# Kernel optimization log

Hardware: AMD Instinct MI355X
Metric: run time of the kernel (lower is better)

The kernel has to match this reference:

```python
import jax, jax.numpy as jnp
import numpy as np

N = 100000
E = 1600000
D = 128
L = 3  # num_layers
EPS = 1e-5


def setup_inputs() -> dict:
    key = jax.random.key(0)
    ks = jax.random.split(key, 10)
    feat = jax.random.normal(ks[0], (N, D), dtype=jnp.float32)
    src = jax.random.randint(ks[1], (E,), 0, N, dtype=jnp.int32)
    dst = jax.random.randint(ks[2], (E,), 0, N, dtype=jnp.int32)
    s = 1.0 / np.sqrt(D)
    W_pool = jax.random.uniform(ks[3], (L, D, D), jnp.float32, -s, s)
    b_pool = jax.random.uniform(ks[4], (L, D), jnp.float32, -s, s)
    W_self = jax.random.uniform(ks[5], (L, D, D), jnp.float32, -s, s)
    W_neigh = jax.random.uniform(ks[6], (L, D, D), jnp.float32, -s, s)
    bias = jnp.zeros((L, D), jnp.float32)
    gamma = jnp.ones((L, D), jnp.float32)
    beta = jnp.zeros((L, D), jnp.float32)
    return {"feat": feat, "W_pool": W_pool, "b_pool": b_pool, "W_self": W_self,
            "W_neigh": W_neigh, "bias": bias, "gamma": gamma, "beta": beta,
            "src": src, "dst": dst}


def _sage_pool_layer(h, Wp, bp, Ws, Wn, b, src_all, dst_all):
    # DGL SAGEConv(aggregator_type='pool'):
    # h_pool = relu(fc_pool(h)); neigh = max over in-edges of h_pool[src];
    # out = fc_self(h) + fc_neigh(neigh) + bias  (fc_self/fc_neigh bias-free)
    hp = jax.nn.relu(h @ Wp + bp)                      # [N, d]
    msgs = hp[src_all]                                  # [E+N, d] gather
    neigh = jax.ops.segment_max(msgs, dst_all, num_segments=N)  # [N, d]
    return h @ Ws + neigh @ Wn + b


def _bn_relu(x, g, b):
    # BatchNorm1d in training mode (batch stats, biased variance) + ReLU
    mean = jnp.mean(x, axis=0)
    var = jnp.mean(jnp.square(x - mean), axis=0)
    return jax.nn.relu((x - mean) * jax.lax.rsqrt(var + EPS) * g + b)


def reference(feat, W_pool, b_pool, W_self, W_neigh, bias, gamma, beta, src, dst):
    # dgl.add_self_loop
    loop = jnp.arange(N, dtype=src.dtype)
    src_all = jnp.concatenate([src, loop])
    dst_all = jnp.concatenate([dst, loop])
    h = feat
    for l in range(L):
        h = _sage_pool_layer(h, W_pool[l], b_pool[l], W_self[l], W_neigh[l],
                             bias[l], src_all, dst_all)
        h = _bn_relu(h, gamma[l], beta[l])
    return h
```

## Files before the change

### kernel.cpp

```cpp
#include <hip/hip_runtime.h>

#define DD 128
#define MAXB 256
#define BSH 9
#define PEB 4096
#define RB 64
#define CAP 10240

typedef unsigned short u16;
typedef unsigned int   u32;
typedef __attribute__((ext_vector_type(8))) short bf16x8;
typedef __attribute__((ext_vector_type(4))) float f32x4;

union U8 { uint4 u; bf16x8 v; };

__device__ inline u16 f2bf(float x) {
  u32 u = __float_as_uint(x);
  u += 0x7fffu + ((u >> 16) & 1u);
  return (u16)(u >> 16);
}
__device__ inline float bf2f_lo(u32 w) { return __uint_as_float(w << 16); }
__device__ inline float bf2f_hi(u32 w) { return __uint_as_float(w & 0xffff0000u); }

__device__ inline u32 pkmax(u32 a, u32 b) {
  u32 r;
  asm("v_pk_max_u16 %0, %1, %2" : "=v"(r) : "v"(a), "v"(b));
  return r;
}

__device__ inline uint4 fragF32(const float* __restrict__ p) {
  float4 a = *(const float4*)p;
  float4 b = *(const float4*)(p + 4);
  uint4 o;
  o.x = (u32)f2bf(a.x) | ((u32)f2bf(a.y) << 16);
  o.y = (u32)f2bf(a.z) | ((u32)f2bf(a.w) << 16);
  o.z = (u32)f2bf(b.x) | ((u32)f2bf(b.y) << 16);
  o.w = (u32)f2bf(b.z) | ((u32)f2bf(b.w) << 16);
  return o;
}

__device__ inline uint4 fragBN(const u16* __restrict__ p,
                               const float* __restrict__ sc,
                               const float* __restrict__ sh, int k0) {
  uint4 u = *(const uint4*)p;
  float4 c0 = *(const float4*)(sc + k0);
  float4 c1 = *(const float4*)(sc + k0 + 4);
  float4 h0 = *(const float4*)(sh + k0);
  float4 h1 = *(const float4*)(sh + k0 + 4);
  float y0 = fmaxf(fmaf(bf2f_lo(u.x), c0.x, h0.x), 0.f);
  float y1 = fmaxf(fmaf(bf2f_hi(u.x), c0.y, h0.y), 0.f);
  float y2 = fmaxf(fmaf(bf2f_lo(u.y), c0.z, h0.z), 0.f);
  float y3 = fmaxf(fmaf(bf2f_hi(u.y), c0.w, h0.w), 0.f);
  float y4 = fmaxf(fmaf(bf2f_lo(u.z), c1.x, h1.x), 0.f);
  float y5 = fmaxf(fmaf(bf2f_hi(u.z), c1.y, h1.y), 0.f);
  float y6 = fmaxf(fmaf(bf2f_lo(u.w), c1.z, h1.z), 0.f);
  float y7 = fmaxf(fmaf(bf2f_hi(u.w), c1.w, h1.w), 0.f);
  uint4 o;
  o.x = (u32)f2bf(y0) | ((u32)f2bf(y1) << 16);
  o.y = (u32)f2bf(y2) | ((u32)f2bf(y3) << 16);
  o.z = (u32)f2bf(y4) | ((u32)f2bf(y5) << 16);
  o.w = (u32)f2bf(y6) | ((u32)f2bf(y7) << 16);
  return o;
}

__global__ __launch_bounds__(256) void k_pack_w(
    const float* __restrict__ Wp, const float* __restrict__ Wsf,
    const float* __restrict__ Wn, u16* __restrict__ Wpk)
{
  int g = blockIdx.x * 256 + threadIdx.x;
  int m = g >> 11;
  if (m >= 9) return;
  int t = g & 2047;
  const float* W = (m < 3) ? Wp + (size_t)m * 16384
                 : (m < 6) ? Wsf + (size_t)(m - 3) * 16384
                           : Wn + (size_t)(m - 6) * 16384;
  int ks = t >> 9, nt = (t >> 6) & 7, l = t & 63;
  int kbase = ks * 32 + (l >> 4) * 8;
  int n = nt * 16 + (l & 15);
  u32 o[4];
#pragma unroll
  for (int p = 0; p < 4; p++) {
    u16 e0 = f2bf(W[(size_t)(kbase + 2 * p) * DD + n]);
    u16 e1 = f2bf(W[(size_t)(kbase + 2 * p + 1) * DD + n]);
    o[p] = (u32)e0 | ((u32)e1 << 16);
  }
  uint4* dst = (uint4*)(Wpk + (size_t)m * 16384 + (size_t)t * 8);
  *dst = make_uint4(o[0], o[1], o[2], o[3]);
}

template<int MODE>
__global__ __launch_bounds__(256, 4) void k_gemm_pool(
    const float* __restrict__ featf, const u16* __restrict__ xb,
    const u16* __restrict__ Wpk, const float* __restrict__ bvec,
    const float* __restrict__ sc, const float* __restrict__ sh,
    u16* __restrict__ hp, int nrows)
{
  const int tid = threadIdx.x;
  const int w = tid >> 6, l = tid & 63;
  const int lg = l >> 4, lm = l & 15;
  const int m0 = blockIdx.x * 128 + w * 32;

  f32x4 acc[2][8];
#pragma unroll
  for (int a = 0; a < 2; a++)
#pragma unroll
    for (int b = 0; b < 8; b++) acc[a][b] = (f32x4){0.f, 0.f, 0.f, 0.f};

  int n0 = m0 + lm;      if (n0 >= nrows) n0 = nrows - 1;
  int n1 = m0 + 16 + lm; if (n1 >= nrows) n1 = nrows - 1;
  const u16* wl = Wpk + l * 8;

#pragma unroll
  for (int ks = 0; ks < 4; ks++) {
    const int k0 = ks * 32 + lg * 8;
    U8 a0, a1;
    if (MODE == 0) {
      a0.u = fragF32(featf + (size_t)n0 * DD + k0);
      a1.u = fragF32(featf + (size_t)n1 * DD + k0);
    } else {
      a0.u = fragBN(xb + (size_t)n0 * DD + k0, sc, sh, k0);
      a1.u = fragBN(xb + (size_t)n1 * DD + k0, sc, sh, k0);
    }
#pragma unroll
    for (int nt = 0; nt < 8; nt++) {
      bf16x8 wf = *(const bf16x8*)(wl + (ks * 8 + nt) * 512);
      acc[0][nt] = __builtin_amdgcn_mfma_f32_16x16x32_bf16(wf, a0.v, acc[0][nt], 0, 0, 0);
      acc[1][nt] = __builtin_amdgcn_mfma_f32_16x16x32_bf16(wf, a1.v, acc[1][nt], 0, 0, 0);
    }
  }

#pragma unroll
  for (int mf = 0; mf < 2; mf++) {
    int node = m0 + mf * 16 + lm;
    if (node < nrows) {
      u16* dst = hp + (size_t)node * DD + lg * 4;
#pragma unroll
      for (int nt = 0; nt < 8; nt++) {
        float4 b4 = *(const float4*)(bvec + nt * 16 + lg * 4);
        f32x4 a = acc[mf][nt];
        float v0 = fmaxf(a[0] + b4.x, 0.f);
        float v1 = fmaxf(a[1] + b4.y, 0.f);
        float v2 = fmaxf(a[2] + b4.z, 0.f);
        float v3 = fmaxf(a[3] + b4.w, 0.f);
        uint2 o;
        o.x = (u32)f2bf(v0) | ((u32)f2bf(v1) << 16);
        o.y = (u32)f2bf(v2) | ((u32)f2bf(v3) << 16);
        *(uint2*)(dst + nt * 16) = o;
      }
    }
  }
}

template<int MODE>
__global__ __launch_bounds__(256, 4) void k_gemm_out(
    const float* __restrict__ featf, u16* xb,
    const u16* __restrict__ gb,
    const u16* __restrict__ WpkS, const u16* __restrict__ WpkN,
    const float* __restrict__ bvec,
    const float* __restrict__ sc, const float* __restrict__ sh,
    float* __restrict__ parts, int nrows)
{
  __shared__ float red[64 * 132];
  const int tid = threadIdx.x;
  const int w = tid >> 6, l = tid & 63;
  const int lg = l >> 4, lm = l & 15;
  const int m0 = blockIdx.x * 128 + w * 32;

  f32x4 acc[2][8];
#pragma unroll
  for (int a = 0; a < 2; a++)
#pragma unroll
    for (int b = 0; b < 8; b++) acc[a][b] = (f32x4){0.f, 0.f, 0.f, 0.f};

  int n0 = m0 + lm;      if (n0 >= nrows) n0 = nrows - 1;
  int n1 = m0 + 16 + lm; if (n1 >= nrows) n1 = nrows - 1;

#pragma unroll
  for (int ks = 0; ks < 4; ks++) {
    const int k0 = ks * 32 + lg * 8;
    U8 a0, a1;
    if (MODE == 0) {
      a0.u = fragF32(featf + (size_t)n0 * DD + k0);
      a1.u = fragF32(featf + (size_t)n1 * DD + k0);
    } else {
      a0.u = fragBN(xb + (size_t)n0 * DD + k0, sc, sh, k0);
      a1.u = fragBN(xb + (size_t)n1 * DD + k0, sc, sh, k0);
    }
    const u16* wl = WpkS + l * 8;
#pragma unroll
    for (int nt = 0; nt < 8; nt++) {
      bf16x8 wf = *(const bf16x8*)(wl + (ks * 8 + nt) * 512);
      acc[0][nt] = __builtin_amdgcn_mfma_f32_16x16x32_bf16(wf, a0.v, acc[0][nt], 0, 0, 0);
      acc[1][nt] = __builtin_amdgcn_mfma_f32_16x16x32_bf16(wf, a1.v, acc[1][nt], 0, 0, 0);
    }
  }
#pragma unroll
  for (int ks = 0; ks < 4; ks++) {
    const int k0 = ks * 32 + lg * 8;
    bf16x8 g0 = *(const bf16x8*)(gb + (size_t)n0 * DD + k0);
    bf16x8 g1 = *(const bf16x8*)(gb + (size_t)n1 * DD + k0);
    const u16* wl = WpkN + l * 8;
#pragma unroll
    for (int nt = 0; nt < 8; nt++) {
      bf16x8 wf = *(const bf16x8*)(wl + (ks * 8 + nt) * 512);
      acc[0][nt] = __builtin_amdgcn_mfma_f32_16x16x32_bf16(wf, g0, acc[0][nt], 0, 0, 0);
      acc[1][nt] = __builtin_amdgcn_mfma_f32_16x16x32_bf16(wf, g1, acc[1][nt], 0, 0, 0);
    }
  }

  const float msk0 = (m0 + lm < nrows) ? 1.f : 0.f;
  const float msk1 = (m0 + 16 + lm < nrows) ? 1.f : 0.f;
#pragma unroll
  for (int nt = 0; nt < 8; nt++) {
    float4 b4 = *(const float4*)(bvec + nt * 16 + lg * 4);
    acc[0][nt][0] += b4.x; acc[0][nt][1] += b4.y;
    acc[0][nt][2] += b4.z; acc[0][nt][3] += b4.w;
    acc[1][nt][0] += b4.x; acc[1][nt][1] += b4.y;
    acc[1][nt][2] += b4.z; acc[1][nt][3] += b4.w;
  }
#pragma unroll
  for (int mf = 0; mf < 2; mf++) {
    int node = m0 + mf * 16 + lm;
    if (node < nrows) {
      u16* dst = xb + (size_t)node * DD + lg * 4;
#pragma unroll
      for (int nt = 0; nt < 8; nt++) {
        f32x4 a = acc[mf][nt];
        uint2 o;
        o.x = (u32)f2bf(a[0]) | ((u32)f2bf(a[1]) << 16);
        o.y = (u32)f2bf(a[2]) | ((u32)f2bf(a[3]) << 16);
        *(uint2*)(dst + nt * 16) = o;
      }
    }
  }

  const int rowbase = (w * 16 + lm) * 132;
#pragma unroll
  for (int nt = 0; nt < 8; nt++) {
    float4 sv;
    sv.x = msk0 * acc[0][nt][0] + msk1 * acc[1][nt][0];
    sv.y = msk0 * acc[0][nt][1] + msk1 * acc[1][nt][1];
    sv.z = msk0 * acc[0][nt][2] + msk1 * acc[1][nt][2];
    sv.w = msk0 * acc[0][nt][3] + msk1 * acc[1][nt][3];
    *(float4*)&red[rowbase + nt * 16 + lg * 4] = sv;
  }
  __syncthreads();
  float ssum = 0.f;
  if (tid < 128) {
#pragma unroll
    for (int r = 0; r < 64; r++) ssum += red[r * 132 + tid];
  }
  __syncthreads();
#pragma unroll
  for (int nt = 0; nt < 8; nt++) {
    float4 qv;
    qv.x = msk0 * acc[0][nt][0] * acc[0][nt][0] + msk1 * acc[1][nt][0] * acc[1][nt][0];
    qv.y = msk0 * acc[0][nt][1] * acc[0][nt][1] + msk1 * acc[1][nt][1] * acc[1][nt][1];
    qv.z = msk0 * acc[0][nt][2] * acc[0][nt][2] + msk1 * acc[1][nt][2] * acc[1][nt][2];
    qv.w = msk0 * acc[0][nt][3] * acc[0][nt][3] + msk1 * acc[1][nt][3] * acc[1][nt][3];
    *(float4*)&red[rowbase + nt * 16 + lg * 4] = qv;
  }
  __syncthreads();
  if (tid < 128) {
    float qsum = 0.f;
#pragma unroll
    for (int r = 0; r < 64; r++) qsum += red[r * 132 + tid];
    parts[(size_t)blockIdx.x * 256 + tid] = ssum;
    parts[(size_t)blockIdx.x * 256 + 128 + tid] = qsum;
  }
}

__global__ __launch_bounds__(256) void k_red1(
    const float* __restrict__ parts, float* __restrict__ pp, int nblk)
{
  int t = threadIdx.x;
  float s = 0.f;
  for (int r = blockIdx.x; r < nblk; r += RB) s += parts[(size_t)r * 256 + t];
  pp[blockIdx.x * 256 + t] = s;
}

__global__ void k_init(int* __restrict__ bcur, int* __restrict__ bcnt) {
  int i = threadIdx.x;
  bcur[i] = i * CAP;
  bcnt[i] = 0;
}

__global__ __launch_bounds__(256) void k_part(
    const int* __restrict__ src, const int* __restrict__ dst,
    int* __restrict__ bcur, int* __restrict__ bcnt,
    u32* __restrict__ pairs, int E)
{
  __shared__ int cnt[MAXB];
  __shared__ int base[MAXB];
  const int e0 = blockIdx.x * PEB;
  const int e1 = min(e0 + PEB, E);
  for (int i = threadIdx.x; i < MAXB; i += 256) cnt[i] = 0;
  __syncthreads();
  for (int e = e0 + threadIdx.x; e < e1; e += 256)
    atomicAdd(&cnt[dst[e] >> BSH], 1);
  __syncthreads();
  for (int i = threadIdx.x; i < MAXB; i += 256) {
    int c = cnt[i];
    if (c) { base[i] = atomicAdd(&bcur[i], c); atomicAdd(&bcnt[i], c); }
    cnt[i] = 0;
  }
  __syncthreads();
  for (int e = e0 + threadIdx.x; e < e1; e += 256) {
    int d = dst[e], s = src[e];
    int b = d >> BSH;
    int r = atomicAdd(&cnt[b], 1);
    pairs[base[b] + r] = ((u32)s << 9) | (u32)(d & 511);
  }
}

__global__ __launch_bounds__(256) void k_csr(
    const u32* __restrict__ pairs, const int* __restrict__ bcnt,
    int* __restrict__ off, int* __restrict__ endv,
    int* __restrict__ eidx, int nrows)
{
  __shared__ int cnt[512];
  __shared__ int ps[256];
  const int b = blockIdx.x;
  const int lo = b * CAP;
  const int hi = lo + bcnt[b];
  const int t = threadIdx.x;
  cnt[t] = 0; cnt[t + 256] = 0;
  __syncthreads();
  for (int i = lo + t; i < hi; i += 256)
    atomicAdd(&cnt[pairs[i] & 511], 1);
  __syncthreads();
  int c0 = cnt[2 * t], c1 = cnt[2 * t + 1];
  ps[t] = c0 + c1;
  __syncthreads();
  int acc = ps[t];
#pragma unroll
  for (int s = 1; s < 256; s <<= 1) {
    int u = (t >= s) ? ps[t - s] : 0;
    __syncthreads();
    acc += u;
    ps[t] = acc;
    __syncthreads();
  }
  int base = lo + acc - (c0 + c1);
  int node0 = (b << BSH) + 2 * t;
  if (node0 < nrows)     { off[node0]     = base;      endv[node0]     = base + c0; }
  if (node0 + 1 < nrows) { off[node0 + 1] = base + c0; endv[node0 + 1] = base + c0 + c1; }
  cnt[2 * t]     = base;
  cnt[2 * t + 1] = base + c0;
  __syncthreads();
  for (int i = lo + t; i < hi; i += 256) {
    u32 p = pairs[i];
    int pos = atomicAdd(&cnt[p & 511], 1);
    eidx[pos] = (int)(p >> 9);
  }
}

__global__ __launch_bounds__(256) void k_aggregate(
    const uint4* __restrict__ hp4, const int* __restrict__ off,
    const int* __restrict__ endv, const int* __restrict__ eidx,
    uint4* __restrict__ nb4, int nrows)
{
  int d = blockIdx.x * 4 + (threadIdx.x >> 6);
  if (d >= nrows) return;
  const int l = threadIdx.x & 63;
  const int part = l & 15;
  const int slot = l >> 4;
  uint4 a = hp4[(size_t)d * 16 + part];
  const int b = off[d], e = endv[d];
  const int len = (e - b + 3) >> 2;
  int i = b + slot * len;
  const int i1 = min(i + len, e);
  for (; i + 3 < i1; i += 4) {
    int s0 = eidx[i], s1 = eidx[i + 1], s2 = eidx[i + 2], s3 = eidx[i + 3];
    uint4 v0 = hp4[(size_t)s0 * 16 + part];
    uint4 v1 = hp4[(size_t)s1 * 16 + part];
    uint4 v2 = hp4[(size_t)s2 * 16 + part];
    uint4 v3 = hp4[(size_t)s3 * 16 + part];
    a.x = pkmax(pkmax(a.x, pkmax(v0.x, v1.x)), pkmax(v2.x, v3.x));
    a.y = pkmax(pkmax(a.y, pkmax(v0.y, v1.y)), pkmax(v2.y, v3.y));
    a.z = pkmax(pkmax(a.z, pkmax(v0.z, v1.z)), pkmax(v2.z, v3.z));
    a.w = pkmax(pkmax(a.w, pkmax(v0.w, v1.w)), pkmax(v2.w, v3.w));
  }
  if (i < i1) {
    int s0 = eidx[i];
    int s1 = (i + 1 < i1) ? eidx[i + 1] : s0;
    int s2 = (i + 2 < i1) ? eidx[i + 2] : s0;
    uint4 v0 = hp4[(size_t)s0 * 16 + part];
    uint4 v1 = hp4[(size_t)s1 * 16 + part];
    uint4 v2 = hp4[(size_t)s2 * 16 + part];
    a.x = pkmax(pkmax(a.x, v0.x), pkmax(v1.x, v2.x));
    a.y = pkmax(pkmax(a.y, v0.y), pkmax(v1.y, v2.y));
    a.z = pkmax(pkmax(a.z, v0.z), pkmax(v1.z, v2.z));
    a.w = pkmax(pkmax(a.w, v0.w), pkmax(v1.w, v2.w));
  }
  a.x = pkmax(a.x, (u32)__shfl_xor((int)a.x, 16, 64));
  a.y = pkmax(a.y, (u32)__shfl_xor((int)a.y, 16, 64));
  a.z = pkmax(a.z, (u32)__shfl_xor((int)a.z, 16, 64));
  a.w = pkmax(a.w, (u32)__shfl_xor((int)a.w, 16, 64));
  a.x = pkmax(a.x, (u32)__shfl_xor((int)a.x, 32, 64));
  a.y = pkmax(a.y, (u32)__shfl_xor((int)a.y, 32, 64));
  a.z = pkmax(a.z, (u32)__shfl_xor((int)a.z, 32, 64));
  a.w = pkmax(a.w, (u32)__shfl_xor((int)a.w, 32, 64));
  if (slot == 0) nb4[(size_t)d * 16 + part] = a;
}

__global__ __launch_bounds__(256) void k_bn_prep(
    const float* __restrict__ pp,
    const float* __restrict__ gamma, const float* __restrict__ beta,
    float* __restrict__ sc, float* __restrict__ sh, float invN)
{
  __shared__ float sums[256];
  int t = threadIdx.x;
  float s = 0.f;
#pragma unroll
  for (int k = 0; k < RB; k++) s += pp[k * 256 + t];
  sums[t] = s;
  __syncthreads();
  if (t < 128) {
    float mean = sums[t] * invN;
    float var  = sums[128 + t] * invN - mean * mean;
    float g = gamma[t] * rsqrtf(var + 1e-5f);
    sc[t] = g;
    sh[t] = beta[t] - mean * g;
  }
}

__global__ __launch_bounds__(256) void k_bn_final(
    const u16* __restrict__ xb, float* __restrict__ out,
    const float* __restrict__ sc, const float* __restrict__ sh, int n8)
{
  int i = blockIdx.x * 256 + threadIdx.x;
  if (i >= n8) return;
  uint4 v = ((const uint4*)xb)[i];
  int f0 = (i & 15) * 8;
  float4 c0 = *(const float4*)(sc + f0);
  float4 c1 = *(const float4*)(sc + f0 + 4);
  float4 h0 = *(const float4*)(sh + f0);
  float4 h1 = *(const float4*)(sh + f0 + 4);
  float4* o = (float4*)out + 2 * (size_t)i;
  o[0] = make_float4(fmaxf(fmaf(bf2f_lo(v.x), c0.x, h0.x), 0.f),
                     fmaxf(fmaf(bf2f_hi(v.x), c0.y, h0.y), 0.f),
                     fmaxf(fmaf(bf2f_lo(v.y), c0.z, h0.z), 0.f),
                     fmaxf(fmaf(bf2f_hi(v.y), c0.w, h0.w), 0.f));
  o[1] = make_float4(fmaxf(fmaf(bf2f_lo(v.z), c1.x, h1.x), 0.f),
                     fmaxf(fmaf(bf2f_hi(v.z), c1.y, h1.y), 0.f),
                     fmaxf(fmaf(bf2f_lo(v.w), c1.z, h1.z), 0.f),
                     fmaxf(fmaf(bf2f_hi(v.w), c1.w, h1.w), 0.f));
}

extern "C" void kernel_launch(void* const* d_in, const int* in_sizes, int n_in,
                              void* d_out, int out_size, void* d_ws, size_t ws_size,
                              hipStream_t stream)
{
  const float* feat    = (const float*)d_in[0];
  const float* W_pool  = (const float*)d_in[1];
  const float* b_pool  = (const float*)d_in[2];
  const float* W_self  = (const float*)d_in[3];
  const float* W_neigh = (const float*)d_in[4];
  const float* bias    = (const float*)d_in[5];
  const float* gamma   = (const float*)d_in[6];
  const float* beta    = (const float*)d_in[7];
  const int*   src     = (const int*)d_in[8];
  const int*   dst     = (const int*)d_in[9];

  const int Nn = in_sizes[0] / DD;
  const int E  = in_sizes[8];
  float* out = (float*)d_out;

  const int gB = (Nn + 127) / 128;

  const size_t ND = (size_t)Nn * DD;
  u16*   xb    = (u16*)d_ws;
  u16*   hp    = xb + ND;
  u16*   nbuf  = hp + ND;
  u16*   Wpk   = nbuf + ND;
  float* sc    = (float*)(Wpk + 9 * 16384);
  float* sh    = sc + 128;
  float* pp    = sh + 128;
  float* parts = pp + RB * 256;
  int*   bcnt  = (int*)(parts + (size_t)gB * 256);
  int*   bcur  = bcnt + MAXB;
  int*   off   = bcur + MAXB;
  int*   endv  = off + Nn;
  const int nbuk = (Nn + 511) >> BSH;
  u32*   pairs = (u32*)(endv + Nn);
  int*   eidx  = (int*)(pairs + (size_t)nbuk * CAP);

  const int pB   = (E + PEB - 1) / PEB;
  const int aggB = (Nn + 3) / 4;
  const int n8   = Nn * (DD / 8);
  const int cB   = (n8 + 255) / 256;

  k_pack_w<<<72, 256, 0, stream>>>(W_pool, W_self, W_neigh, Wpk);
  k_init<<<1, MAXB, 0, stream>>>(bcur, bcnt);
  k_part<<<pB, 256, 0, stream>>>(src, dst, bcur, bcnt, pairs, E);
  k_csr<<<nbuk, 256, 0, stream>>>(pairs, bcnt, off, endv, eidx, Nn);

  for (int l = 0; l < 3; l++) {
    const float* bp = b_pool + (size_t)l * DD;
    const float* bl = bias + (size_t)l * DD;
    const u16* WP = Wpk + (size_t)l * 16384;
    const u16* WS = Wpk + (size_t)(3 + l) * 16384;
    const u16* WN = Wpk + (size_t)(6 + l) * 16384;

    if (l == 0)
      k_gemm_pool<0><<<gB, 256, 0, stream>>>(feat, nullptr, WP, bp, sc, sh, hp, Nn);
    else
      k_gemm_pool<1><<<gB, 256, 0, stream>>>(nullptr, xb, WP, bp, sc, sh, hp, Nn);

    k_aggregate<<<aggB, 256, 0, stream>>>((const uint4*)hp, off, endv, eidx, (uint4*)nbuf, Nn);

    if (l == 0)
      k_gemm_out<0><<<gB, 256, 0, stream>>>(feat, xb, nbuf, WS, WN, bl, sc, sh, parts, Nn);
    else
      k_gemm_out<1><<<gB, 256, 0, stream>>>(nullptr, xb, nbuf, WS, WN, bl, sc, sh, parts, Nn);

    k_red1<<<RB, 256, 0, stream>>>(parts, pp, gB);
    k_bn_prep<<<1, 256, 0, stream>>>(pp, gamma + (size_t)l * DD,
                                     beta + (size_t)l * DD, sc, sh, 1.0f / (float)Nn);
  }
  k_bn_final<<<cB, 256, 0, stream>>>(xb, out, sc, sh, n8);
  (void)n_in; (void)out_size; (void)ws_size;
}
```

Before: 435.5 us.

## Register-cache edge loads in partition, pack CSR offsets, raise occupancy bounds

The partition kernel now loads its 16 src/dst values per thread into registers once and reuses them in both the counting and the scatter passes, so dst is no longer read from global memory twice. The CSR offset and end arrays are merged into one int2 array, so aggregation reads both bounds with a single load. Launch-bounds occupancy hints are raised for the pool GEMM (4 to 6) and the aggregate kernel (8). This trades register budget for more waves in flight, which may cause spills in the GEMM.

```diff
diff --git a/kernel.cpp b/kernel.cpp
--- a/kernel.cpp
+++ b/kernel.cpp
@@ -89,7 +89,7 @@
 }
 
 template<int MODE>
-__global__ __launch_bounds__(256, 4) void k_gemm_pool(
+__global__ __launch_bounds__(256, 6) void k_gemm_pool(
     const float* __restrict__ featf, const u16* __restrict__ xb,
     const u16* __restrict__ Wpk, const float* __restrict__ bvec,
     const float* __restrict__ sc, const float* __restrict__ sh,
@@ -293,11 +293,19 @@
   __shared__ int cnt[MAXB];
   __shared__ int base[MAXB];
   const int e0 = blockIdx.x * PEB;
-  const int e1 = min(e0 + PEB, E);
+  int s[16], d[16];
+#pragma unroll
+  for (int k = 0; k < 16; k++) {
+    int e = e0 + threadIdx.x + k * 256;
+    bool ok = (e < E);
+    s[k] = ok ? src[e] : 0;
+    d[k] = ok ? dst[e] : -1;
+  }
   for (int i = threadIdx.x; i < MAXB; i += 256) cnt[i] = 0;
   __syncthreads();
-  for (int e = e0 + threadIdx.x; e < e1; e += 256)
-    atomicAdd(&cnt[dst[e] >> BSH], 1);
+#pragma unroll
+  for (int k = 0; k < 16; k++)
+    if (d[k] >= 0) atomicAdd(&cnt[d[k] >> BSH], 1);
   __syncthreads();
   for (int i = threadIdx.x; i < MAXB; i += 256) {
     int c = cnt[i];
@@ -305,18 +313,19 @@
     cnt[i] = 0;
   }
   __syncthreads();
-  for (int e = e0 + threadIdx.x; e < e1; e += 256) {
-    int d = dst[e], s = src[e];
-    int b = d >> BSH;
-    int r = atomicAdd(&cnt[b], 1);
-    pairs[base[b] + r] = ((u32)s << 9) | (u32)(d & 511);
+#pragma unroll
+  for (int k = 0; k < 16; k++) {
+    if (d[k] >= 0) {
+      int b = d[k] >> BSH;
+      int r = atomicAdd(&cnt[b], 1);
+      pairs[base[b] + r] = ((u32)s[k] << 9) | (u32)(d[k] & 511);
+    }
   }
 }
 
 __global__ __launch_bounds__(256) void k_csr(
     const u32* __restrict__ pairs, const int* __restrict__ bcnt,
-    int* __restrict__ off, int* __restrict__ endv,
-    int* __restrict__ eidx, int nrows)
+    int2* __restrict__ offend, int* __restrict__ eidx, int nrows)
 {
   __shared__ int cnt[512];
   __shared__ int ps[256];
@@ -343,8 +352,8 @@
   }
   int base = lo + acc - (c0 + c1);
   int node0 = (b << BSH) + 2 * t;
-  if (node0 < nrows)     { off[node0]     = base;      endv[node0]     = base + c0; }
-  if (node0 + 1 < nrows) { off[node0 + 1] = base + c0; endv[node0 + 1] = base + c0 + c1; }
+  if (node0 < nrows)     offend[node0]     = make_int2(base, base + c0);
+  if (node0 + 1 < nrows) offend[node0 + 1] = make_int2(base + c0, base + c0 + c1);
   cnt[2 * t]     = base;
   cnt[2 * t + 1] = base + c0;
   __syncthreads();
@@ -355,10 +364,9 @@
   }
 }
 
-__global__ __launch_bounds__(256) void k_aggregate(
-    const uint4* __restrict__ hp4, const int* __restrict__ off,
-    const int* __restrict__ endv, const int* __restrict__ eidx,
-    uint4* __restrict__ nb4, int nrows)
+__global__ __launch_bounds__(256, 8) void k_aggregate(
+    const uint4* __restrict__ hp4, const int2* __restrict__ offend,
+    const int* __restrict__ eidx, uint4* __restrict__ nb4, int nrows)
 {
   int d = blockIdx.x * 4 + (threadIdx.x >> 6);
   if (d >= nrows) return;
@@ -366,7 +374,8 @@
   const int part = l & 15;
   const int slot = l >> 4;
   uint4 a = hp4[(size_t)d * 16 + part];
-  const int b = off[d], e = endv[d];
+  const int2 oe = offend[d];
+  const int b = oe.x, e = oe.y;
   const int len = (e - b + 3) >> 2;
   int i = b + slot * len;
   const int i1 = min(i + len, e);
@@ -480,10 +489,9 @@
   float* parts = pp + RB * 256;
   int*   bcnt  = (int*)(parts + (size_t)gB * 256);
   int*   bcur  = bcnt + MAXB;
-  int*   off   = bcur + MAXB;
-  int*   endv  = off + Nn;
+  int2*  offend = (int2*)(bcur + MAXB);
   const int nbuk = (Nn + 511) >> BSH;
-  u32*   pairs = (u32*)(endv + Nn);
+  u32*   pairs = (u32*)(offend + Nn);
   int*   eidx  = (int*)(pairs + (size_t)nbuk * CAP);
 
   const int pB   = (E + PEB - 1) / PEB;
@@ -494,7 +502,7 @@
   k_pack_w<<<72, 256, 0, stream>>>(W_pool, W_self, W_neigh, Wpk);
   k_init<<<1, MAXB, 0, stream>>>(bcur, bcnt);
   k_part<<<pB, 256, 0, stream>>>(src, dst, bcur, bcnt, pairs, E);
-  k_csr<<<nbuk, 256, 0, stream>>>(pairs, bcnt, off, endv, eidx, Nn);
+  k_csr<<<nbuk, 256, 0, stream>>>(pairs, bcnt, offend, eidx, Nn);
 
   for (int l = 0; l < 3; l++) {
     const float* bp = b_pool + (size_t)l * DD;
@@ -508,7 +516,7 @@
     else
       k_gemm_pool<1><<<gB, 256, 0, stream>>>(nullptr, xb, WP, bp, sc, sh, hp, Nn);
 
-    k_aggregate<<<aggB, 256, 0, stream>>>((const uint4*)hp, off, endv, eidx, (uint4*)nbuf, Nn);
+    k_aggregate<<<aggB, 256, 0, stream>>>((const uint4*)hp, offend, eidx, (uint4*)nbuf, Nn);
 
     if (l == 0)
       k_gemm_out<0><<<gB, 256, 0, stream>>>(feat, xb, nbuf, WS, WN, bl, sc, sh, parts, Nn);
```

After: 488.7 us. 1.12x slower.
